# Kernel optimization log

Measured on AMD Instinct MI355X. Metric: run time of the kernel, lower is better.

## Reference

```python
import jax, jax.numpy as jnp
import numpy as np
import math

D_K = 64
DROP_P = 0.5

def setup_inputs() -> dict:
    key = jax.random.key(0)
    kq, kk, kv, km = jax.random.split(key, 4)
    B, S, d = 32, 2048, D_K
    Q = jax.random.normal(kq, (B, S, d), dtype=jnp.float32)
    K = jax.random.normal(kk, (B, S, d), dtype=jnp.float32)
    V = jax.random.normal(kv, (B, S, d), dtype=jnp.float32)
    # Bernoulli(keep_prob) mask for training-mode dropout (p=0.5)
    dropout_mask = jax.random.bernoulli(km, 1.0 - DROP_P, (B, S, S))
    return {"Q": Q, "K": K, "V": V, "dropout_mask": dropout_mask}

def reference(Q, K, V, dropout_mask):
    # attn = softmax(Q K^T / sqrt(d_k)); dropout; y = attn V
    scale = 1.0 / math.sqrt(D_K)
    scores = jnp.einsum('bqd,bkd->bqk', Q, K) * scale   # [B,S,S]
    attn = jax.nn.softmax(scores, axis=-1)
    keep_scale = 1.0 / (1.0 - DROP_P)
    attn = jnp.where(dropout_mask, attn * keep_scale, 0.0)
    y = jnp.einsum('bqk,bkd->bqd', attn, V)             # [B,S,d]
    return (y, attn)
```

## Files before the change

kernel.cpp:

```cpp
#include <hip/hip_runtime.h>
#include <hip/hip_bf16.h>
#include <stdint.h>

#define SQ 2048
#define DK 64
#define NB 32
#define TQ 16
#define EW 2064
#define NTHREADS 512
#define SCL 0.18033688011112042f

typedef __attribute__((ext_vector_type(8))) short short8;
typedef __attribute__((ext_vector_type(4))) float f32x4;
typedef __attribute__((ext_vector_type(4))) unsigned u32x4;
typedef __attribute__((ext_vector_type(2))) unsigned u32x2;

__device__ __forceinline__ unsigned f2bf_u(float x) {
    unsigned u = __builtin_bit_cast(unsigned, x);
    u += 0x7fffu + ((u >> 16) & 1u);
    return u >> 16;
}
__device__ __forceinline__ float bf2f(unsigned h) {
    return __builtin_bit_cast(float, h << 16);
}
__device__ __forceinline__ void split8(const float* p, short8& h, short8& l) {
    f32x4 a = *(const f32x4*)p;
    f32x4 b = *(const f32x4*)(p + 4);
    #pragma unroll
    for (int j = 0; j < 4; ++j) {
        unsigned ua = f2bf_u(a[j]);
        h[j] = (short)ua; l[j] = (short)f2bf_u(a[j] - bf2f(ua));
        unsigned ub = f2bf_u(b[j]);
        h[j + 4] = (short)ub; l[j + 4] = (short)f2bf_u(b[j] - bf2f(ub));
    }
}
__device__ __forceinline__ unsigned pkf16(float a, float b) {
    unsigned short ha = __builtin_bit_cast(unsigned short, (_Float16)a);
    unsigned short hb = __builtin_bit_cast(unsigned short, (_Float16)b);
    return (unsigned)ha | ((unsigned)hb << 16);
}
__device__ __forceinline__ float upk16(unsigned u, int hi) {
    return (float)__builtin_bit_cast(_Float16, (unsigned short)(hi ? (u >> 16) : (u & 0xffffu)));
}

__global__ __launch_bounds__(256) void prep_kernel(
    const float* __restrict__ K, const float* __restrict__ V,
    unsigned short* __restrict__ Khi, unsigned short* __restrict__ Klo,
    unsigned short* __restrict__ Vt)
{
    __shared__ float vtile[64][65];
    const int t  = threadIdx.x;
    const int b  = blockIdx.x >> 5;
    const int s0 = (blockIdx.x & 31) << 6;
    const size_t base = ((size_t)b * SQ + s0) * DK + (size_t)t * 16;

    {
        short8 h0, l0, h1, l1;
        split8(K + base,     h0, l0);
        split8(K + base + 8, h1, l1);
        *(short8*)(Khi + base)     = h0;
        *(short8*)(Khi + base + 8) = h1;
        *(short8*)(Klo + base)     = l0;
        *(short8*)(Klo + base + 8) = l1;
    }
    {
        const int sr = t >> 2, dc = (t & 3) << 4;
        #pragma unroll
        for (int u = 0; u < 16; u += 4) {
            f32x4 v = *(const f32x4*)(V + base + u);
            vtile[sr][dc + u + 0] = v[0];
            vtile[sr][dc + u + 1] = v[1];
            vtile[sr][dc + u + 2] = v[2];
            vtile[sr][dc + u + 3] = v[3];
        }
    }
    __syncthreads();
    #pragma unroll
    for (int rep = 0; rep < 16; ++rep) {
        const int idx = rep * 256 + t;
        const int d = idx >> 6, s = idx & 63;
        Vt[((size_t)b * DK + d) * SQ + s0 + s] = (unsigned short)f2bf_u(vtile[s][d]);
    }
}

__global__ __launch_bounds__(NTHREADS, 4) void sdpa_main(
    const float* __restrict__ Q, const unsigned short* __restrict__ Khi,
    const unsigned short* __restrict__ Klo, const unsigned short* __restrict__ Vt,
    const unsigned* __restrict__ Mk, float* __restrict__ Yout, float* __restrict__ Aout)
{
    __shared__ __align__(16) unsigned short e_lds[TQ][EW];
    __shared__ float yp[4][TQ][16];
    __shared__ float rsum[8][TQ];
    __shared__ float i2s[TQ];

    const int tid  = threadIdx.x;
    const int lane = tid & 63;
    const int wv   = tid >> 6;
    const int m16  = lane & 15;
    const int kq   = lane >> 4;
    const int koff = kq * 8;

    const int b  = blockIdx.x >> 7;
    const int q0 = (blockIdx.x & 127) * TQ;

    short8 qh[2], ql[2];
    {
        const float* qrow = Q + ((size_t)b * SQ + q0 + m16) * DK;
        split8(qrow + koff,      qh[0], ql[0]);
        split8(qrow + 32 + koff, qh[1], ql[1]);
    }

    float rs = 0.f;
    {
        const size_t krow = ((size_t)b * SQ + wv * 256 + m16) * DK;
        const unsigned short* khp = Khi + krow;
        const unsigned short* klp = Klo + krow;
        const int xw = (m16 & 7) << 3;
        for (int t = 0; t < 16; ++t) {
            const int off = t * 16 * DK;
            f32x4 acc = {0.f, 0.f, 0.f, 0.f};
            #pragma unroll
            for (int c = 0; c < 2; ++c) {
                short8 kh = *(const short8*)(khp + off + c * 32 + koff);
                short8 kl = *(const short8*)(klp + off + c * 32 + koff);
                acc = __builtin_amdgcn_mfma_f32_16x16x32_bf16(kh, qh[c], acc, 0, 0, 0);
                acc = __builtin_amdgcn_mfma_f32_16x16x32_bf16(kh, ql[c], acc, 0, 0, 0);
                acc = __builtin_amdgcn_mfma_f32_16x16x32_bf16(kl, qh[c], acc, 0, 0, 0);
            }
            const float e0 = exp2f(acc[0] * SCL);
            const float e1 = exp2f(acc[1] * SCL);
            const float e2 = exp2f(acc[2] * SCL);
            const float e3 = exp2f(acc[3] * SCL);
            rs += (e0 + e1) + (e2 + e3);
            u32x2 pk;
            pk[0] = pkf16(e0, e1);
            pk[1] = pkf16(e2, e3);
            *(u32x2*)&e_lds[m16][(wv * 256 + t * 16 + kq * 4) ^ xw] = pk;
        }
    }
    rs += __shfl_xor(rs, 16);
    rs += __shfl_xor(rs, 32);
    if (lane < 16) rsum[wv][lane] = rs;
    __syncthreads();
    if (tid < 16) {
        float s = 0.f;
        #pragma unroll
        for (int w = 0; w < 8; ++w) s += rsum[w][tid];
        i2s[tid] = 2.0f / s;
    }
    __syncthreads();

    const int cr = tid >> 5;
    const int cc = (tid & 31) * 8;
    const int xc = (cr & 7) << 3;
    const float i2 = i2s[cr];
    const size_t crow = ((size_t)b * SQ + q0 + cr) * SQ + cc;

    const int g   = wv >> 1;
    const int par = wv & 1;
    const int xm  = (m16 & 7) << 3;
    const unsigned short* vrow = Vt + ((size_t)b * DK + g * 16 + m16) * SQ;
    f32x4 acc = {0.f, 0.f, 0.f, 0.f};

    #define C_FINISH(s, ma, mb)                                                   \
    {                                                                             \
        unsigned short* ep = &e_lds[cr][((s) * 256 + cc) ^ xc];                   \
        const u32x4 ev = *(const u32x4*)ep;                                       \
        const float a0 = (ma)[0] ? upk16(ev[0], 0) * i2 : 0.f;                    \
        const float a1 = (ma)[1] ? upk16(ev[0], 1) * i2 : 0.f;                    \
        const float a2 = (ma)[2] ? upk16(ev[1], 0) * i2 : 0.f;                    \
        const float a3 = (ma)[3] ? upk16(ev[1], 1) * i2 : 0.f;                    \
        const float a4 = (mb)[0] ? upk16(ev[2], 0) * i2 : 0.f;                    \
        const float a5 = (mb)[1] ? upk16(ev[2], 1) * i2 : 0.f;                    \
        const float a6 = (mb)[2] ? upk16(ev[3], 0) * i2 : 0.f;                    \
        const float a7 = (mb)[3] ? upk16(ev[3], 1) * i2 : 0.f;                    \
        f32x4 av0 = {a0, a1, a2, a3};                                             \
        f32x4 av1 = {a4, a5, a6, a7};                                             \
        __builtin_nontemporal_store(av0, (f32x4*)(Aout + crow + (s) * 256));      \
        __builtin_nontemporal_store(av1, (f32x4*)(Aout + crow + (s) * 256 + 4));  \
        u32x4 pb;                                                                 \
        pb[0] = f2bf_u(a0) | (f2bf_u(a1) << 16);                                  \
        pb[1] = f2bf_u(a2) | (f2bf_u(a3) << 16);                                  \
        pb[2] = f2bf_u(a4) | (f2bf_u(a5) << 16);                                  \
        pb[3] = f2bf_u(a6) | (f2bf_u(a7) << 16);                                  \
        *(u32x4*)ep = pb;                                                         \
    }

    {
        u32x4 ma = __builtin_nontemporal_load((const u32x4*)(Mk + crow));
        u32x4 mb = __builtin_nontemporal_load((const u32x4*)(Mk + crow + 4));
        C_FINISH(0, ma, mb);
    }
    __syncthreads();

    for (int s = 0; s < 8; ++s) {
        u32x4 na, nb;
        if (s < 7) {
            na = __builtin_nontemporal_load((const u32x4*)(Mk + crow + (s + 1) * 256));
            nb = __builtin_nontemporal_load((const u32x4*)(Mk + crow + (s + 1) * 256 + 4));
        }
        #pragma unroll
        for (int c = 0; c < 4; ++c) {
            const int k0 = s * 256 + par * 128 + c * 32;
            short8 af = *(const short8*)&e_lds[m16][(k0 + koff) ^ xm];
            short8 vf = *(const short8*)(vrow + k0 + koff);
            acc = __builtin_amdgcn_mfma_f32_16x16x32_bf16(af, vf, acc, 0, 0, 0);
        }
        if (s < 7) C_FINISH(s + 1, na, nb);
        __syncthreads();
    }

    if (par == 1) {
        #pragma unroll
        for (int r = 0; r < 4; ++r) yp[g][kq * 4 + r][m16] = acc[r];
    }
    __syncthreads();
    if (par == 0) {
        #pragma unroll
        for (int r = 0; r < 4; ++r) {
            const float yv = acc[r] + yp[g][kq * 4 + r][m16];
            __builtin_nontemporal_store(yv,
                Yout + ((size_t)b * SQ + q0 + kq * 4 + r) * DK + g * 16 + m16);
        }
    }
    #undef C_FINISH
}

extern "C" void kernel_launch(void* const* d_in, const int* in_sizes, int n_in,
                              void* d_out, int out_size, void* d_ws, size_t ws_size,
                              hipStream_t stream) {
    const float*    Q  = (const float*)d_in[0];
    const float*    K  = (const float*)d_in[1];
    const float*    V  = (const float*)d_in[2];
    const unsigned* Mk = (const unsigned*)d_in[3];
    float* Yout = (float*)d_out;
    float* Aout = (float*)d_out + (size_t)NB * SQ * DK;

    const size_t NEL = (size_t)NB * SQ * DK;
    unsigned short* Khi = (unsigned short*)d_ws;
    unsigned short* Klo = Khi + NEL;
    unsigned short* Vt  = Klo + NEL;

    prep_kernel<<<dim3(NB * (SQ / 64)), dim3(256), 0, stream>>>(K, V, Khi, Klo, Vt);
    sdpa_main<<<dim3(NB * (SQ / TQ)), dim3(NTHREADS), 0, stream>>>(
        Q, Khi, Klo, Vt, Mk, Yout, Aout);
}
```

Before: 498.6 us.

## Deepen dropout-mask prefetch to two stripes and use lighter LDS-only barriers

Loads of the dropout mask for the first two stripes are issued at kernel start, before the QK^T phase, and the mask loop becomes a fully unrolled double-buffered pipeline that prefetches two stripes ahead. __syncthreads is replaced by an explicit lgkmcnt wait plus s_barrier, so the barrier does not wait on outstanding global loads. The aim is to hide mask load latency behind compute. The cost is more live registers, which can lower occupancy.

```diff
diff --git a/kernel.cpp b/kernel.cpp
--- a/kernel.cpp
+++ b/kernel.cpp
@@ -102,6 +102,16 @@
 
     const int b  = blockIdx.x >> 7;
     const int q0 = (blockIdx.x & 127) * TQ;
+
+    const int cr = tid >> 5;
+    const int cc = (tid & 31) * 8;
+    const int xc = (cr & 7) << 3;
+    const size_t crow = ((size_t)b * SQ + q0 + cr) * SQ + cc;
+
+    u32x4 ma0 = __builtin_nontemporal_load((const u32x4*)(Mk + crow));
+    u32x4 mb0 = __builtin_nontemporal_load((const u32x4*)(Mk + crow + 4));
+    u32x4 ma1 = __builtin_nontemporal_load((const u32x4*)(Mk + crow + 256));
+    u32x4 mb1 = __builtin_nontemporal_load((const u32x4*)(Mk + crow + 256 + 4));
 
     short8 qh[2], ql[2];
     {
@@ -150,11 +160,7 @@
     }
     __syncthreads();
 
-    const int cr = tid >> 5;
-    const int cc = (tid & 31) * 8;
-    const int xc = (cr & 7) << 3;
     const float i2 = i2s[cr];
-    const size_t crow = ((size_t)b * SQ + q0 + cr) * SQ + cc;
 
     const int g   = wv >> 1;
     const int par = wv & 1;
@@ -186,29 +192,42 @@
         *(u32x4*)ep = pb;                                                         \
     }
 
-    {
-        u32x4 ma = __builtin_nontemporal_load((const u32x4*)(Mk + crow));
-        u32x4 mb = __builtin_nontemporal_load((const u32x4*)(Mk + crow + 4));
-        C_FINISH(0, ma, mb);
-    }
-    __syncthreads();
-
-    for (int s = 0; s < 8; ++s) {
-        u32x4 na, nb;
-        if (s < 7) {
-            na = __builtin_nontemporal_load((const u32x4*)(Mk + crow + (s + 1) * 256));
-            nb = __builtin_nontemporal_load((const u32x4*)(Mk + crow + (s + 1) * 256 + 4));
-        }
-        #pragma unroll
-        for (int c = 0; c < 4; ++c) {
-            const int k0 = s * 256 + par * 128 + c * 32;
-            short8 af = *(const short8*)&e_lds[m16][(k0 + koff) ^ xm];
-            short8 vf = *(const short8*)(vrow + k0 + koff);
-            acc = __builtin_amdgcn_mfma_f32_16x16x32_bf16(af, vf, acc, 0, 0, 0);
-        }
-        if (s < 7) C_FINISH(s + 1, na, nb);
-        __syncthreads();
-    }
+    #define PV_STRIPE(s)                                                          \
+    {                                                                             \
+        _Pragma("unroll")                                                         \
+        for (int c = 0; c < 4; ++c) {                                             \
+            const int k0 = (s) * 256 + par * 128 + c * 32;                        \
+            short8 af = *(const short8*)&e_lds[m16][(k0 + koff) ^ xm];            \
+            short8 vf = *(const short8*)(vrow + k0 + koff);                       \
+            acc = __builtin_amdgcn_mfma_f32_16x16x32_bf16(af, vf, acc, 0, 0, 0);  \
+        }                                                                         \
+    }
+
+    #define CBAR()                                                                \
+        asm volatile("s_waitcnt lgkmcnt(0)" ::: "memory");                        \
+        __builtin_amdgcn_s_barrier();                                             \
+        __builtin_amdgcn_sched_barrier(0);
+
+    #define REFILL(slotA, slotB, s)                                               \
+        slotA = __builtin_nontemporal_load((const u32x4*)(Mk + crow + (s) * 256));\
+        slotB = __builtin_nontemporal_load((const u32x4*)(Mk + crow + (s) * 256 + 4));
+
+    C_FINISH(0, ma0, mb0);
+    CBAR();
+
+    REFILL(ma0, mb0, 2); PV_STRIPE(0); C_FINISH(1, ma1, mb1); CBAR();
+    REFILL(ma1, mb1, 3); PV_STRIPE(1); C_FINISH(2, ma0, mb0); CBAR();
+    REFILL(ma0, mb0, 4); PV_STRIPE(2); C_FINISH(3, ma1, mb1); CBAR();
+    REFILL(ma1, mb1, 5); PV_STRIPE(3); C_FINISH(4, ma0, mb0); CBAR();
+    REFILL(ma0, mb0, 6); PV_STRIPE(4); C_FINISH(5, ma1, mb1); CBAR();
+    REFILL(ma1, mb1, 7); PV_STRIPE(5); C_FINISH(6, ma0, mb0); CBAR();
+                         PV_STRIPE(6); C_FINISH(7, ma1, mb1); CBAR();
+                         PV_STRIPE(7);
+
+    #undef REFILL
+    #undef CBAR
+    #undef PV_STRIPE
+    #undef C_FINISH
 
     if (par == 1) {
         #pragma unroll
@@ -223,7 +242,6 @@
                 Yout + ((size_t)b * SQ + q0 + kq * 4 + r) * DK + g * 16 + m16);
         }
     }
-    #undef C_FINISH
 }
 
 extern "C" void kernel_launch(void* const* d_in, const int* in_sizes, int n_in,
```

Measured after the change: 499.2 us. No clear change (+0.1%).

## Split key dimension across two blocks, recompute row sums, reduce Y partials separately

Applied to the files above, without the earlier changes.

Each query tile is now handled by two blocks, each owning half of the key range. Both blocks recompute the full QK^T to get the softmax denominator, but only the owned half is kept in LDS. The dropout mask is applied during the exp stage and stored as bf16 instead of fp16. The LDS footprint is halved so occupancy can double (launch bounds 4->8), the per-stripe syncthreads loop is removed, and partial Y outputs go through a workspace and a new reduction kernel. In exchange, the QK^T MFMA and exp work is doubled and an extra kernel launch plus a Y round-trip through global memory are added.

```diff
diff --git a/kernel.cpp b/kernel.cpp
--- a/kernel.cpp
+++ b/kernel.cpp
@@ -6,7 +6,7 @@
 #define DK 64
 #define NB 32
 #define TQ 16
-#define EW 2064
+#define KH 1024
 #define NTHREADS 512
 #define SCL 0.18033688011112042f
 
@@ -22,6 +22,9 @@
 }
 __device__ __forceinline__ float bf2f(unsigned h) {
     return __builtin_bit_cast(float, h << 16);
+}
+__device__ __forceinline__ float bf2f_hi(unsigned u) {
+    return __builtin_bit_cast(float, u & 0xffff0000u);
 }
 __device__ __forceinline__ void split8(const float* p, short8& h, short8& l) {
     f32x4 a = *(const f32x4*)p;
@@ -33,14 +36,6 @@
         unsigned ub = f2bf_u(b[j]);
         h[j + 4] = (short)ub; l[j + 4] = (short)f2bf_u(b[j] - bf2f(ub));
     }
-}
-__device__ __forceinline__ unsigned pkf16(float a, float b) {
-    unsigned short ha = __builtin_bit_cast(unsigned short, (_Float16)a);
-    unsigned short hb = __builtin_bit_cast(unsigned short, (_Float16)b);
-    return (unsigned)ha | ((unsigned)hb << 16);
-}
-__device__ __forceinline__ float upk16(unsigned u, int hi) {
-    return (float)__builtin_bit_cast(_Float16, (unsigned short)(hi ? (u >> 16) : (u & 0xffffu)));
 }
 
 __global__ __launch_bounds__(256) void prep_kernel(
@@ -83,12 +78,12 @@
     }
 }
 
-__global__ __launch_bounds__(NTHREADS, 4) void sdpa_main(
+__global__ __launch_bounds__(NTHREADS, 8) void sdpa_main(
     const float* __restrict__ Q, const unsigned short* __restrict__ Khi,
     const unsigned short* __restrict__ Klo, const unsigned short* __restrict__ Vt,
-    const unsigned* __restrict__ Mk, float* __restrict__ Yout, float* __restrict__ Aout)
+    const unsigned* __restrict__ Mk, float* __restrict__ Yp, float* __restrict__ Aout)
 {
-    __shared__ __align__(16) unsigned short e_lds[TQ][EW];
+    __shared__ __align__(16) unsigned short e_half[TQ][KH];
     __shared__ float yp[4][TQ][16];
     __shared__ float rsum[8][TQ];
     __shared__ float i2s[TQ];
@@ -100,8 +95,13 @@
     const int kq   = lane >> 4;
     const int koff = kq * 8;
 
-    const int b  = blockIdx.x >> 7;
-    const int q0 = (blockIdx.x & 127) * TQ;
+    const int bx = blockIdx.x;
+    const int b  = bx >> 8;
+    const int qt = (bx >> 1) & 127;
+    const int kh = bx & 1;
+    const int q0 = qt * TQ;
+    const int wlocal = wv & 3;
+    const bool owned = (wv >> 2) == kh;
 
     short8 qh[2], ql[2];
     {
@@ -116,26 +116,51 @@
         const unsigned short* khp = Khi + krow;
         const unsigned short* klp = Klo + krow;
         const int xw = (m16 & 7) << 3;
-        for (int t = 0; t < 16; ++t) {
-            const int off = t * 16 * DK;
-            f32x4 acc = {0.f, 0.f, 0.f, 0.f};
-            #pragma unroll
-            for (int c = 0; c < 2; ++c) {
-                short8 kh = *(const short8*)(khp + off + c * 32 + koff);
-                short8 kl = *(const short8*)(klp + off + c * 32 + koff);
-                acc = __builtin_amdgcn_mfma_f32_16x16x32_bf16(kh, qh[c], acc, 0, 0, 0);
-                acc = __builtin_amdgcn_mfma_f32_16x16x32_bf16(kh, ql[c], acc, 0, 0, 0);
-                acc = __builtin_amdgcn_mfma_f32_16x16x32_bf16(kl, qh[c], acc, 0, 0, 0);
+
+        if (owned) {
+            const unsigned* mrow = Mk + ((size_t)b * SQ + q0 + m16) * SQ
+                                 + (size_t)kh * KH + wlocal * 256 + kq * 4;
+            for (int t = 0; t < 16; ++t) {
+                const int off = t * 16 * DK;
+                f32x4 acc = {0.f, 0.f, 0.f, 0.f};
+                #pragma unroll
+                for (int c = 0; c < 2; ++c) {
+                    short8 k_h = *(const short8*)(khp + off + c * 32 + koff);
+                    short8 k_l = *(const short8*)(klp + off + c * 32 + koff);
+                    acc = __builtin_amdgcn_mfma_f32_16x16x32_bf16(k_h, qh[c], acc, 0, 0, 0);
+                    acc = __builtin_amdgcn_mfma_f32_16x16x32_bf16(k_h, ql[c], acc, 0, 0, 0);
+                    acc = __builtin_amdgcn_mfma_f32_16x16x32_bf16(k_l, qh[c], acc, 0, 0, 0);
+                }
+                const u32x4 m = __builtin_nontemporal_load((const u32x4*)(mrow + t * 16));
+                const float e0 = exp2f(acc[0] * SCL);
+                const float e1 = exp2f(acc[1] * SCL);
+                const float e2 = exp2f(acc[2] * SCL);
+                const float e3 = exp2f(acc[3] * SCL);
+                rs += (e0 + e1) + (e2 + e3);
+                const float a0 = m[0] ? e0 : 0.f;
+                const float a1 = m[1] ? e1 : 0.f;
+                const float a2 = m[2] ? e2 : 0.f;
+                const float a3 = m[3] ? e3 : 0.f;
+                u32x2 pk;
+                pk[0] = f2bf_u(a0) | (f2bf_u(a1) << 16);
+                pk[1] = f2bf_u(a2) | (f2bf_u(a3) << 16);
+                *(u32x2*)&e_half[m16][(wlocal * 256 + t * 16 + kq * 4) ^ xw] = pk;
             }
-            const float e0 = exp2f(acc[0] * SCL);
-            const float e1 = exp2f(acc[1] * SCL);
-            const float e2 = exp2f(acc[2] * SCL);
-            const float e3 = exp2f(acc[3] * SCL);
-            rs += (e0 + e1) + (e2 + e3);
-            u32x2 pk;
-            pk[0] = pkf16(e0, e1);
-            pk[1] = pkf16(e2, e3);
-            *(u32x2*)&e_lds[m16][(wv * 256 + t * 16 + kq * 4) ^ xw] = pk;
+        } else {
+            for (int t = 0; t < 16; ++t) {
+                const int off = t * 16 * DK;
+                f32x4 acc = {0.f, 0.f, 0.f, 0.f};
+                #pragma unroll
+                for (int c = 0; c < 2; ++c) {
+                    short8 k_h = *(const short8*)(khp + off + c * 32 + koff);
+                    short8 k_l = *(const short8*)(klp + off + c * 32 + koff);
+                    acc = __builtin_amdgcn_mfma_f32_16x16x32_bf16(k_h, qh[c], acc, 0, 0, 0);
+                    acc = __builtin_amdgcn_mfma_f32_16x16x32_bf16(k_h, ql[c], acc, 0, 0, 0);
+                    acc = __builtin_amdgcn_mfma_f32_16x16x32_bf16(k_l, qh[c], acc, 0, 0, 0);
+                }
+                rs += (exp2f(acc[0] * SCL) + exp2f(acc[1] * SCL))
+                    + (exp2f(acc[2] * SCL) + exp2f(acc[3] * SCL));
+            }
         }
     }
     rs += __shfl_xor(rs, 16);
@@ -154,76 +179,67 @@
     const int cc = (tid & 31) * 8;
     const int xc = (cr & 7) << 3;
     const float i2 = i2s[cr];
-    const size_t crow = ((size_t)b * SQ + q0 + cr) * SQ + cc;
+    const size_t arow = ((size_t)b * SQ + q0 + cr) * SQ + (size_t)kh * KH + cc;
 
     const int g   = wv >> 1;
     const int par = wv & 1;
     const int xm  = (m16 & 7) << 3;
-    const unsigned short* vrow = Vt + ((size_t)b * DK + g * 16 + m16) * SQ;
+    const unsigned short* vbase = Vt + ((size_t)b * DK + g * 16 + m16) * SQ + (size_t)kh * KH;
     f32x4 acc = {0.f, 0.f, 0.f, 0.f};
 
-    #define C_FINISH(s, ma, mb)                                                   \
+    #define CSTRIPE(s)                                                            \
     {                                                                             \
-        unsigned short* ep = &e_lds[cr][((s) * 256 + cc) ^ xc];                   \
-        const u32x4 ev = *(const u32x4*)ep;                                       \
-        const float a0 = (ma)[0] ? upk16(ev[0], 0) * i2 : 0.f;                    \
-        const float a1 = (ma)[1] ? upk16(ev[0], 1) * i2 : 0.f;                    \
-        const float a2 = (ma)[2] ? upk16(ev[1], 0) * i2 : 0.f;                    \
-        const float a3 = (ma)[3] ? upk16(ev[1], 1) * i2 : 0.f;                    \
-        const float a4 = (mb)[0] ? upk16(ev[2], 0) * i2 : 0.f;                    \
-        const float a5 = (mb)[1] ? upk16(ev[2], 1) * i2 : 0.f;                    \
-        const float a6 = (mb)[2] ? upk16(ev[3], 0) * i2 : 0.f;                    \
-        const float a7 = (mb)[3] ? upk16(ev[3], 1) * i2 : 0.f;                    \
-        f32x4 av0 = {a0, a1, a2, a3};                                             \
-        f32x4 av1 = {a4, a5, a6, a7};                                             \
-        __builtin_nontemporal_store(av0, (f32x4*)(Aout + crow + (s) * 256));      \
-        __builtin_nontemporal_store(av1, (f32x4*)(Aout + crow + (s) * 256 + 4));  \
-        u32x4 pb;                                                                 \
-        pb[0] = f2bf_u(a0) | (f2bf_u(a1) << 16);                                  \
-        pb[1] = f2bf_u(a2) | (f2bf_u(a3) << 16);                                  \
-        pb[2] = f2bf_u(a4) | (f2bf_u(a5) << 16);                                  \
-        pb[3] = f2bf_u(a6) | (f2bf_u(a7) << 16);                                  \
-        *(u32x4*)ep = pb;                                                         \
-    }
-
-    {
-        u32x4 ma = __builtin_nontemporal_load((const u32x4*)(Mk + crow));
-        u32x4 mb = __builtin_nontemporal_load((const u32x4*)(Mk + crow + 4));
-        C_FINISH(0, ma, mb);
-    }
-    __syncthreads();
-
-    for (int s = 0; s < 8; ++s) {
-        u32x4 na, nb;
-        if (s < 7) {
-            na = __builtin_nontemporal_load((const u32x4*)(Mk + crow + (s + 1) * 256));
-            nb = __builtin_nontemporal_load((const u32x4*)(Mk + crow + (s + 1) * 256 + 4));
+        const u32x4 ev = *(const u32x4*)&e_half[cr][((s) * 256 + cc) ^ xc];       \
+        f32x4 o0, o1;                                                             \
+        o0[0] = bf2f(ev[0] & 0xffffu) * i2;  o0[1] = bf2f_hi(ev[0]) * i2;         \
+        o0[2] = bf2f(ev[1] & 0xffffu) * i2;  o0[3] = bf2f_hi(ev[1]) * i2;         \
+        o1[0] = bf2f(ev[2] & 0xffffu) * i2;  o1[1] = bf2f_hi(ev[2]) * i2;         \
+        o1[2] = bf2f(ev[3] & 0xffffu) * i2;  o1[3] = bf2f_hi(ev[3]) * i2;         \
+        __builtin_nontemporal_store(o0, (f32x4*)(Aout + arow + (s) * 256));       \
+        __builtin_nontemporal_store(o1, (f32x4*)(Aout + arow + (s) * 256 + 4));   \
+    }
+    #define PVCHUNK4(c0)                                                          \
+    {                                                                             \
+        _Pragma("unroll")                                                         \
+        for (int c = (c0); c < (c0) + 4; ++c) {                                   \
+            const int kl = par * 512 + c * 32;                                    \
+            short8 af = *(const short8*)&e_half[m16][(kl + koff) ^ xm];           \
+            short8 vf = *(const short8*)(vbase + kl + koff);                      \
+            acc = __builtin_amdgcn_mfma_f32_16x16x32_bf16(af, vf, acc, 0, 0, 0);  \
+        }                                                                         \
+    }
+
+    CSTRIPE(0) PVCHUNK4(0)
+    CSTRIPE(1) PVCHUNK4(4)
+    CSTRIPE(2) PVCHUNK4(8)
+    CSTRIPE(3) PVCHUNK4(12)
+
+    #undef PVCHUNK4
+    #undef CSTRIPE
+
+    if (par == 1) {
+        #pragma unroll
+        for (int r = 0; r < 4; ++r) yp[g][kq * 4 + r][m16] = acc[r];
+    }
+    __syncthreads();
+    if (par == 0) {
+        #pragma unroll
+        for (int r = 0; r < 4; ++r) {
+            const float yv = (acc[r] + yp[g][kq * 4 + r][m16]) * i2s[kq * 4 + r];
+            Yp[((size_t)(kh * NB + b) * SQ + q0 + kq * 4 + r) * DK + g * 16 + m16] = yv;
         }
-        #pragma unroll
-        for (int c = 0; c < 4; ++c) {
-            const int k0 = s * 256 + par * 128 + c * 32;
-            short8 af = *(const short8*)&e_lds[m16][(k0 + koff) ^ xm];
-            short8 vf = *(const short8*)(vrow + k0 + koff);
-            acc = __builtin_amdgcn_mfma_f32_16x16x32_bf16(af, vf, acc, 0, 0, 0);
-        }
-        if (s < 7) C_FINISH(s + 1, na, nb);
-        __syncthreads();
-    }
-
-    if (par == 1) {
-        #pragma unroll
-        for (int r = 0; r < 4; ++r) yp[g][kq * 4 + r][m16] = acc[r];
-    }
-    __syncthreads();
-    if (par == 0) {
-        #pragma unroll
-        for (int r = 0; r < 4; ++r) {
-            const float yv = acc[r] + yp[g][kq * 4 + r][m16];
-            __builtin_nontemporal_store(yv,
-                Yout + ((size_t)b * SQ + q0 + kq * 4 + r) * DK + g * 16 + m16);
-        }
-    }
-    #undef C_FINISH
+    }
+}
+
+__global__ __launch_bounds__(256) void yred_kernel(
+    const float* __restrict__ Yp, float* __restrict__ Yout)
+{
+    const size_t NEL = (size_t)NB * SQ * DK;
+    const size_t i = ((size_t)blockIdx.x * 256 + threadIdx.x) * 4;
+    f32x4 a = *(const f32x4*)(Yp + i);
+    f32x4 b = *(const f32x4*)(Yp + NEL + i);
+    f32x4 s = a + b;
+    __builtin_nontemporal_store(s, (f32x4*)(Yout + i));
 }
 
 extern "C" void kernel_launch(void* const* d_in, const int* in_sizes, int n_in,
@@ -240,8 +256,10 @@
     unsigned short* Khi = (unsigned short*)d_ws;
     unsigned short* Klo = Khi + NEL;
     unsigned short* Vt  = Klo + NEL;
+    float*          Yp  = (float*)(Vt + NEL);
 
     prep_kernel<<<dim3(NB * (SQ / 64)), dim3(256), 0, stream>>>(K, V, Khi, Klo, Vt);
-    sdpa_main<<<dim3(NB * (SQ / TQ)), dim3(NTHREADS), 0, stream>>>(
-        Q, Khi, Klo, Vt, Mk, Yout, Aout);
-}
+    sdpa_main<<<dim3(NB * 128 * 2), dim3(NTHREADS), 0, stream>>>(
+        Q, Khi, Klo, Vt, Mk, Yp, Aout);
+    yred_kernel<<<dim3((unsigned)(NEL / 1024)), dim3(256), 0, stream>>>(Yp, Yout);
+}
```

Result: slower. 858.9 us (+72.2%).
